# Performance work log

Hardware: AMD Instinct MI355X
Metric: run time of the kernel (lower is better)

The kernel has to match this reference:

```python
import jax, jax.numpy as jnp
import numpy as np

VOCAB, EMBED, CONT, HID = 829, 8, 40, 32
B, T, CODES = 2048, 256, 32
IN_DIM = EMBED + CONT + 1  # 49: embedding-sum + continuous feats + vanco feedback
SCALE = 1000.0  # all four regularizer scales


def setup_inputs() -> dict:
    key = jax.random.key(0)
    ks = jax.random.split(key, 14)
    s = 1.0 / np.sqrt(HID)
    return {
        "cont": jax.random.normal(ks[0], (B, T, CONT), jnp.float32),
        "cat": jax.random.randint(ks[1], (B, T, CODES), 0, VOCAB),
        "lb": jax.random.uniform(ks[2], (B, T), jnp.float32),
        "dose": jax.random.uniform(ks[3], (B, T), jnp.float32),
        "td": jax.random.uniform(ks[4], (B, T), jnp.float32),
        "v_from_weight": jax.random.uniform(ks[5], (B, T), jnp.float32) + 0.5,
        "vanco_el": jax.random.uniform(ks[6], (B, T), jnp.float32),
        "embed": jax.random.normal(ks[7], (VOCAB, EMBED), jnp.float32) * 0.02,
        "W_ih": jax.random.uniform(ks[8], (3 * HID, IN_DIM), jnp.float32, -s, s),
        "W_hh": jax.random.uniform(ks[9], (3 * HID, HID), jnp.float32, -s, s),
        "b_ih": jax.random.uniform(ks[10], (3 * HID,), jnp.float32, -s, s),
        "b_hh": jax.random.uniform(ks[11], (3 * HID,), jnp.float32, -s, s),
        "W_out": jax.random.uniform(ks[12], (2, HID), jnp.float32, -s, s),
        "b_out": jax.random.uniform(ks[13], (2,), jnp.float32, -s, s),
    }


def _gru_cell(x, h, W_ih, W_hh, b_ih, b_hh):
    gi = x @ W_ih.T + b_ih  # [B, 3H]
    gh = h @ W_hh.T + b_hh
    i_r, i_z, i_n = jnp.split(gi, 3, axis=1)
    h_r, h_z, h_n = jnp.split(gh, 3, axis=1)
    r = jax.nn.sigmoid(i_r + h_r)
    z = jax.nn.sigmoid(i_z + h_z)
    n = jnp.tanh(i_n + r * h_n)
    return (1.0 - z) * n + z * h


def reference(cont, cat, lb, dose, td, v_from_weight, vanco_el,
              embed, W_ih, W_hh, b_ih, b_hh, W_out, b_out):
    dt = cont.dtype
    mask = (lb != 0).astype(dt)  # [B, T]
    # EHR embedding: sum code embeddings per step, concat continuous features
    out_emb = jnp.concatenate([embed[cat].sum(axis=2), cont], axis=2)  # [B, T, 48]
    Bn, Tn = lb.shape
    # feedback uses previous step's mask/label (zeros at step 0)
    fm = jnp.concatenate([jnp.zeros((Bn, 1), dt), mask[:, :-1]], axis=1)
    fl = jnp.concatenate([jnp.zeros((Bn, 1), dt), lb[:, :-1]], axis=1)

    def step(carry, xs):
        h, tm, prev_concn = carry
        e_t, fm_t, fl_t, d_t, td_t = xs
        vfb = jax.lax.stop_gradient(prev_concn) * (1.0 - fm_t) + fl_t * fm_t
        x = jnp.concatenate([e_t, vfb[:, None]], axis=1)  # [B, 49]
        h2 = _gru_cell(x, h, W_ih, W_hh, b_ih, b_hh)
        kv = jnp.exp(h2 @ W_out.T + b_out)  # [B, 2]
        k, v = kv[:, 0], kv[:, 1]
        A = jnp.exp(-k * td_t)
        Bq = (1.0 / k) * (1.0 - jnp.exp(-k * d_t)) * jnp.exp(-k * (td_t - d_t))
        tm2 = tm * A + Bq
        concn = tm2 / (v + 1e-6)
        return (h2, tm2, concn), (concn, k, v)

    init = (jnp.zeros((Bn, HID), dt), jnp.zeros((Bn,), dt), jnp.zeros((Bn,), dt))
    xs = (out_emb.transpose(1, 0, 2), fm.T, fl.T, dose.T, td.T)
    _, (concn, K, V) = jax.lax.scan(step, init, xs)
    output, K, V = concn.T, K.T, V.T  # [B, T]

    kv_change = ((K[:, 1:] - K[:, :-1]) ** 2).mean() * SCALE \
              + ((V[:, 1:] - V[:, :-1]) ** 2).mean() * SCALE
    mse_loss = (((output - lb) * mask) ** 2).sum() / mask.sum()
    K0, V0 = vanco_el[:, 0], v_from_weight[:, 0]
    loss = mse_loss + ((K0 - K[:, 0]) ** 2).mean() * SCALE \
                    + ((V0 - V[:, 0]) ** 2).mean() * SCALE + kv_change
    return (K, V, output, loss, mse_loss)
```

## Files before the change

kernel.cpp:

```cpp
#include <hip/hip_runtime.h>


constexpr int Bn = 2048, Tn = 256;
constexpr int HID = 32, CONT = 40, EMB = 8;
constexpr int VOCAB = 829, CODES = 32;
constexpr int BT = Bn * Tn;
constexpr int LOSS_BLOCKS = 256;

__device__ __forceinline__ float frcp(float x) { return __builtin_amdgcn_rcpf(x); }

__device__ __forceinline__ float swap_add(float x) {
  return x + __shfl_xor(x, 32, 64);
}

template <int CTRL>
__device__ __forceinline__ float dpp_add(float x) {
  int y = __builtin_amdgcn_update_dpp(0, __float_as_int(x), CTRL, 0xf, 0xf, true);
  return x + __int_as_float(y);
}

__global__ __launch_bounds__(256, 2) void rnn_kernel(
    const float* __restrict__ cont, const int* __restrict__ cat,
    const float* __restrict__ lb, const float* __restrict__ dose,
    const float* __restrict__ tdp, const float* __restrict__ embed,
    const float* __restrict__ W_ih, const float* __restrict__ W_hh,
    const float* __restrict__ b_ih, const float* __restrict__ b_hh,
    const float* __restrict__ W_out, const float* __restrict__ b_out,
    float* __restrict__ out) {
  __shared__ __attribute__((aligned(16))) float esh[VOCAB * EMB];
  __shared__ __attribute__((aligned(16))) float ebl[4][64][EMB];
  __shared__ __attribute__((aligned(16))) float hsh[4][HID];

  const int tid = threadIdx.x;
  const int wv = tid >> 6;
  const int j = tid & 63;
  const int u = j & 31;
  const int half = j >> 5;
  const int b = blockIdx.x * 4 + wv;
  const int base = b * Tn;

  for (int i = tid; i < VOCAB * EMB; i += 256) esh[i] = embed[i];
  __syncthreads();

  float wxr[24], wxz[24], wxn[24];
  {
    const float* Wr = W_ih + (size_t)u * 49;
    const float* Wz = W_ih + (size_t)(HID + u) * 49;
    const float* Wn = W_ih + (size_t)(2 * HID + u) * 49;
    const int eo = half * 4;
    const int co = 8 + half * 20;
#pragma unroll
    for (int k = 0; k < 4; k++) { wxr[k] = Wr[eo + k]; wxz[k] = Wz[eo + k]; wxn[k] = Wn[eo + k]; }
#pragma unroll
    for (int k = 0; k < 20; k++) {
      wxr[4 + k] = Wr[co + k]; wxz[4 + k] = Wz[co + k]; wxn[4 + k] = Wn[co + k];
    }
  }
  const float wvr = half ? W_ih[(size_t)u * 49 + 48] : 0.0f;
  const float wvz = half ? W_ih[(size_t)(HID + u) * 49 + 48] : 0.0f;
  const float wvn = half ? W_ih[(size_t)(2 * HID + u) * 49 + 48] : 0.0f;
  float whr[16], whz[16], whn[16];
#pragma unroll
  for (int k = 0; k < 16; k++) {
    whr[k] = W_hh[(size_t)u * HID + half * 16 + k];
    whz[k] = W_hh[(size_t)(HID + u) * HID + half * 16 + k];
    whn[k] = W_hh[(size_t)(2 * HID + u) * HID + half * 16 + k];
  }
  const float br = half ? 0.0f : (b_ih[u] + b_hh[u]);
  const float bz = half ? 0.0f : (b_ih[HID + u] + b_hh[HID + u]);
  const float bni = half ? 0.0f : b_ih[2 * HID + u];
  const float bnh = half ? 0.0f : b_hh[2 * HID + u];
  const float wkv = W_out[half * HID + u];
  const float bo0 = b_out[0], bo1 = b_out[1];

  hsh[wv][u] = 0.0f;
  float hj = 0.0f, tm = 0.0f, concn = 0.0f;
  float td_c = tdp[base], d_c = dose[base], lbp_c = 0.0f;

  float4 xA[5], xB[5];
  {
    const float4* c4 = reinterpret_cast<const float4*>(cont + (size_t)base * CONT + half * 20);
#pragma unroll
    for (int q = 0; q < 5; q++) xA[q] = c4[q];
  }

#define STEP(XC, XN, TT)                                                          \
  {                                                                               \
    const int t = (TT);                                                           \
    const int tn = (t + 1 < Tn) ? (t + 1) : t;                                    \
    {                                              \
      const float4* c4 = reinterpret_cast<const float4*>(                         \
          cont + (size_t)(base + tn) * CONT + half * 20);                         \
      _Pragma("unroll") for (int q = 0; q < 5; q++) XN[q] = c4[q];                \
    }                                                                             \
    const float td_n = tdp[base + tn];                                            \
    const float d_n = dose[base + tn];                                            \
    const float lbp_n = lb[base + tn - 1];                                        \
    const float4 e = *reinterpret_cast<const float4*>(&ebl[wv][t & 63][half * 4]);\
    float ar = wxr[0] * e.x + wxr[1] * e.y + wxr[2] * e.z + wxr[3] * e.w;         \
    float az = wxz[0] * e.x + wxz[1] * e.y + wxz[2] * e.z + wxz[3] * e.w;         \
    float an = wxn[0] * e.x + wxn[1] * e.y + wxn[2] * e.z + wxn[3] * e.w;         \
    _Pragma("unroll") for (int q = 0; q < 5; q++) {                               \
      const float4 xv = XC[q];                                                    \
      const int k0 = 4 + q * 4;                                                   \
      ar += wxr[k0] * xv.x + wxr[k0 + 1] * xv.y + wxr[k0 + 2] * xv.z +            \
            wxr[k0 + 3] * xv.w;                                                   \
      az += wxz[k0] * xv.x + wxz[k0 + 1] * xv.y + wxz[k0 + 2] * xv.z +            \
            wxz[k0 + 3] * xv.w;                                                   \
      an += wxn[k0] * xv.x + wxn[k0 + 1] * xv.y + wxn[k0 + 2] * xv.z +            \
            wxn[k0 + 3] * xv.w;                                                   \
    }                                                                             \
    float gr, gz, gn;                                                             \
    {                                                                             \
      const float4* h4 = reinterpret_cast<const float4*>(&hsh[wv][half * 16]);    \
      const float4 h0 = h4[0];                                                    \
      gr = whr[0] * h0.x + whr[1] * h0.y + whr[2] * h0.z + whr[3] * h0.w;         \
      gz = whz[0] * h0.x + whz[1] * h0.y + whz[2] * h0.z + whz[3] * h0.w;         \
      gn = whn[0] * h0.x + whn[1] * h0.y + whn[2] * h0.z + whn[3] * h0.w;         \
      _Pragma("unroll") for (int q = 1; q < 4; q++) {                             \
        const float4 hv = h4[q];                                                  \
        const int k0 = q * 4;                                                     \
        gr += whr[k0] * hv.x + whr[k0 + 1] * hv.y + whr[k0 + 2] * hv.z +          \
              whr[k0 + 3] * hv.w;                                                 \
        gz += whz[k0] * hv.x + whz[k0 + 1] * hv.y + whz[k0 + 2] * hv.z +          \
              whz[k0 + 3] * hv.w;                                                 \
        gn += whn[k0] * hv.x + whn[k0 + 1] * hv.y + whn[k0 + 2] * hv.z +          \
              whn[k0 + 3] * hv.w;                                                 \
      }                                                                           \
    }                                                                             \
    const float fmv = (lbp_c != 0.0f) ? 1.0f : 0.0f;                              \
    const float vfb = concn * (1.0f - fmv) + lbp_c * fmv;                         \
    ar += vfb * wvr;                                                              \
    az += vfb * wvz;                                                              \
    an += vfb * wvn;                                                              \
    const float sr = swap_add(ar + gr + br);                                      \
    const float sz = swap_add(az + gz + bz);                                      \
    const float sa = swap_add(an + bni);                                          \
    const float sg = swap_add(gn + bnh);                                          \
    const float r = frcp(1.0f + __expf(-sr));                                     \
    const float z = frcp(1.0f + __expf(-sz));                                     \
    const float pre = sa + r * sg;                                                \
    const float nv = 1.0f - 2.0f * frcp(__expf(2.0f * pre) + 1.0f);               \
    const float h2 = (1.0f - z) * nv + z * hj;                                    \
    hsh[wv][u] = h2;                                                              \
    hj = h2;                                                                      \
           \
    float s = h2 * wkv;                                                           \
    s = dpp_add<0x111>(s);                                         \
    s = dpp_add<0x112>(s);                                         \
    s = dpp_add<0x114>(s);                                         \
    s = dpp_add<0x118>(s);                                         \
    s = dpp_add<0x142>(s);  \
    const float pk_s = __int_as_float(__builtin_amdgcn_readlane(__float_as_int(s), 31)); \
    const float pv_s = __int_as_float(__builtin_amdgcn_readlane(__float_as_int(s), 63)); \
    const float kk = __expf(pk_s + bo0);                                          \
    const float vv = __expf(pv_s + bo1);                                          \
    const float Aa = __expf(-kk * td_c);                                          \
    const float eD = __expf(-kk * d_c);                                           \
    const float Bq = frcp(kk) * (1.0f - eD) * __expf(-kk * (td_c - d_c));         \
    tm = tm * Aa + Bq;                                                            \
    concn = tm * frcp(vv + 1e-6f);                                                \
    if (j < 3) {                                                                  \
      const float val = (j == 0) ? kk : ((j == 1) ? vv : concn);                  \
      out[j * BT + base + t] = val;                                               \
    }                                                                             \
    td_c = td_n;                                                                  \
    d_c = d_n;                                                                    \
    lbp_c = lbp_n;                                                                \
  }

  for (int ch = 0; ch < Tn / 64; ++ch) {
    {
      const int4* cp4 =
          reinterpret_cast<const int4*>(cat + ((size_t)(base + ch * 64 + j)) * CODES);
      float a0 = 0.f, a1 = 0.f, a2 = 0.f, a3 = 0.f;
      float a4 = 0.f, a5 = 0.f, a6 = 0.f, a7 = 0.f;
#pragma unroll
      for (int q = 0; q < 8; q++) {
        const int4 c4 = cp4[q];
        {
          const float4* er = reinterpret_cast<const float4*>(esh + c4.x * EMB);
          const float4 r0 = er[0], r1 = er[1];
          a0 += r0.x; a1 += r0.y; a2 += r0.z; a3 += r0.w;
          a4 += r1.x; a5 += r1.y; a6 += r1.z; a7 += r1.w;
        }
        {
          const float4* er = reinterpret_cast<const float4*>(esh + c4.y * EMB);
          const float4 r0 = er[0], r1 = er[1];
          a0 += r0.x; a1 += r0.y; a2 += r0.z; a3 += r0.w;
          a4 += r1.x; a5 += r1.y; a6 += r1.z; a7 += r1.w;
        }
        {
          const float4* er = reinterpret_cast<const float4*>(esh + c4.z * EMB);
          const float4 r0 = er[0], r1 = er[1];
          a0 += r0.x; a1 += r0.y; a2 += r0.z; a3 += r0.w;
          a4 += r1.x; a5 += r1.y; a6 += r1.z; a7 += r1.w;
        }
        {
          const float4* er = reinterpret_cast<const float4*>(esh + c4.w * EMB);
          const float4 r0 = er[0], r1 = er[1];
          a0 += r0.x; a1 += r0.y; a2 += r0.z; a3 += r0.w;
          a4 += r1.x; a5 += r1.y; a6 += r1.z; a7 += r1.w;
        }
      }
      *reinterpret_cast<float4*>(&ebl[wv][j][0]) = make_float4(a0, a1, a2, a3);
      *reinterpret_cast<float4*>(&ebl[wv][j][4]) = make_float4(a4, a5, a6, a7);
    }
    __syncthreads();
#pragma unroll 1
    for (int tl = 0; tl < 64; tl += 2) {
      STEP(xA, xB, ch * 64 + tl);
      STEP(xB, xA, ch * 64 + tl + 1);
    }
  }
#undef STEP
}

__global__ __launch_bounds__(256) void loss_partial_kernel(
    const float* __restrict__ out, const float* __restrict__ lb,
    const float* __restrict__ vel, const float* __restrict__ vfw,
    float* __restrict__ part) {
  float mseN = 0.f, cnt = 0.f, k0 = 0.f, v0 = 0.f, dk = 0.f, dv = 0.f;
  for (int i = blockIdx.x * 256 + threadIdx.x; i < BT; i += LOSS_BLOCKS * 256) {
    const int t = i & (Tn - 1);
    const float l = lb[i];
    const float m = (l != 0.0f) ? 1.0f : 0.0f;
    const float c = out[2 * BT + i];
    const float d = (c - l) * m;
    mseN += d * d;
    cnt += m;
    const float kc = out[i];
    const float vc = out[BT + i];
    if (t > 0) {
      const float kp = out[i - 1];
      const float vp = out[BT + i - 1];
      dk += (kc - kp) * (kc - kp);
      dv += (vc - vp) * (vc - vp);
    } else {
      const float a = vel[i] - kc;
      const float bb = vfw[i] - vc;
      k0 += a * a;
      v0 += bb * bb;
    }
  }
  float acc[6] = {mseN, cnt, k0, v0, dk, dv};
#pragma unroll
  for (int q = 0; q < 6; q++) {
#pragma unroll
    for (int mm = 1; mm < 64; mm <<= 1) acc[q] += __shfl_xor(acc[q], mm, 64);
  }
  __shared__ float red[4][6];
  if ((threadIdx.x & 63) == 0) {
#pragma unroll
    for (int q = 0; q < 6; q++) red[threadIdx.x >> 6][q] = acc[q];
  }
  __syncthreads();
  if (threadIdx.x == 0) {
#pragma unroll
    for (int q = 0; q < 6; q++)
      part[blockIdx.x * 6 + q] = red[0][q] + red[1][q] + red[2][q] + red[3][q];
  }
}

__device__ __forceinline__ void finalize_loss(const float s[6], float* out) {
  const float mse = s[0] / s[1];
  const float loss = mse + (s[2] / (float)Bn) * 1000.0f + (s[3] / (float)Bn) * 1000.0f +
                     (s[4] / (float)(Bn * (Tn - 1))) * 1000.0f +
                     (s[5] / (float)(Bn * (Tn - 1))) * 1000.0f;
  out[3 * BT] = loss;
  out[3 * BT + 1] = mse;
}

__global__ __launch_bounds__(256) void loss_final_kernel(const float* __restrict__ part,
                                                         float* __restrict__ out) {
  float acc[6] = {0.f, 0.f, 0.f, 0.f, 0.f, 0.f};
  for (int i = threadIdx.x; i < LOSS_BLOCKS; i += 256) {
#pragma unroll
    for (int q = 0; q < 6; q++) acc[q] += part[i * 6 + q];
  }
#pragma unroll
  for (int q = 0; q < 6; q++) {
#pragma unroll
    for (int mm = 1; mm < 64; mm <<= 1) acc[q] += __shfl_xor(acc[q], mm, 64);
  }
  __shared__ float red[4][6];
  if ((threadIdx.x & 63) == 0) {
#pragma unroll
    for (int q = 0; q < 6; q++) red[threadIdx.x >> 6][q] = acc[q];
  }
  __syncthreads();
  if (threadIdx.x == 0) {
    float s[6];
#pragma unroll
    for (int q = 0; q < 6; q++) s[q] = red[0][q] + red[1][q] + red[2][q] + red[3][q];
    finalize_loss(s, out);
  }
}

__global__ __launch_bounds__(1024) void loss_single_kernel(
    const float* __restrict__ out, const float* __restrict__ lb,
    const float* __restrict__ vel, const float* __restrict__ vfw,
    float* __restrict__ outw) {
  float mseN = 0.f, cnt = 0.f, k0 = 0.f, v0 = 0.f, dk = 0.f, dv = 0.f;
  for (int i = threadIdx.x; i < BT; i += 1024) {
    const int t = i & (Tn - 1);
    const float l = lb[i];
    const float m = (l != 0.0f) ? 1.0f : 0.0f;
    const float c = out[2 * BT + i];
    const float d = (c - l) * m;
    mseN += d * d;
    cnt += m;
    const float kc = out[i];
    const float vc = out[BT + i];
    if (t > 0) {
      const float kp = out[i - 1];
      const float vp = out[BT + i - 1];
      dk += (kc - kp) * (kc - kp);
      dv += (vc - vp) * (vc - vp);
    } else {
      const float a = vel[i] - kc;
      const float bb = vfw[i] - vc;
      k0 += a * a;
      v0 += bb * bb;
    }
  }
  float acc[6] = {mseN, cnt, k0, v0, dk, dv};
#pragma unroll
  for (int q = 0; q < 6; q++) {
#pragma unroll
    for (int mm = 1; mm < 64; mm <<= 1) acc[q] += __shfl_xor(acc[q], mm, 64);
  }
  __shared__ float red[16][6];
  if ((threadIdx.x & 63) == 0) {
#pragma unroll
    for (int q = 0; q < 6; q++) red[threadIdx.x >> 6][q] = acc[q];
  }
  __syncthreads();
  if (threadIdx.x == 0) {
    float s[6] = {0.f, 0.f, 0.f, 0.f, 0.f, 0.f};
    for (int w = 0; w < 16; w++)
#pragma unroll
      for (int q = 0; q < 6; q++) s[q] += red[w][q];
    finalize_loss(s, outw);
  }
}

extern "C" void kernel_launch(void* const* d_in, const int* in_sizes, int n_in,
                              void* d_out, int out_size, void* d_ws, size_t ws_size,
                              hipStream_t stream) {
  (void)in_sizes; (void)n_in; (void)out_size;
  const float* cont = (const float*)d_in[0];
  const int* cat = (const int*)d_in[1];
  const float* lb = (const float*)d_in[2];
  const float* dose = (const float*)d_in[3];
  const float* tdp = (const float*)d_in[4];
  const float* vfw = (const float*)d_in[5];
  const float* vel = (const float*)d_in[6];
  const float* emb = (const float*)d_in[7];
  const float* W_ih = (const float*)d_in[8];
  const float* W_hh = (const float*)d_in[9];
  const float* b_ih = (const float*)d_in[10];
  const float* b_hh = (const float*)d_in[11];
  const float* W_out = (const float*)d_in[12];
  const float* b_out = (const float*)d_in[13];
  float* out = (float*)d_out;

  rnn_kernel<<<Bn / 4, 256, 0, stream>>>(cont, cat, lb, dose, tdp, emb, W_ih, W_hh,
                                         b_ih, b_hh, W_out, b_out, out);

  if (d_ws != nullptr && ws_size >= (size_t)LOSS_BLOCKS * 6 * sizeof(float)) {
    float* part = (float*)d_ws;
    loss_partial_kernel<<<LOSS_BLOCKS, 256, 0, stream>>>(out, lb, vel, vfw, part);
    loss_final_kernel<<<1, 256, 0, stream>>>(part, out);
  } else {
    loss_single_kernel<<<1, 1024, 0, stream>>>(out, lb, vel, vfw, out);
  }
}
```

Baseline: 237.7 us.

## Deepen input prefetch to two steps and batch per-step outputs through LDS

The recurrent loop now prefetches continuous features and the scalar inputs two timesteps ahead, using four rotating register buffers and a four-step unrolled loop, so global load latency is hidden further behind the serial recurrence. Per-step scalar stores of k, v and concentration from three lanes are replaced by writes into a shared buffer. Each 64-step chunk is then flushed with one coalesced store per output. This adds register pressure under the 2-blocks-per-SM launch bound, plus extra LDS use.

```diff
diff --git a/kernel.cpp b/kernel.cpp
--- a/kernel.cpp
+++ b/kernel.cpp
@@ -30,6 +30,7 @@
   __shared__ __attribute__((aligned(16))) float esh[VOCAB * EMB];
   __shared__ __attribute__((aligned(16))) float ebl[4][64][EMB];
   __shared__ __attribute__((aligned(16))) float hsh[4][HID];
+  __shared__ __attribute__((aligned(16))) float osh[4][3][64];
 
   const int tid = threadIdx.x;
   const int wv = tid >> 6;
@@ -75,33 +76,36 @@
 
   hsh[wv][u] = 0.0f;
   float hj = 0.0f, tm = 0.0f, concn = 0.0f;
+
   float td_c = tdp[base], d_c = dose[base], lbp_c = 0.0f;
-
-  float4 xA[5], xB[5];
+  float td_1 = tdp[base + 1], d_1 = dose[base + 1], lbp_1 = lb[base];
+
+  float4 xA[5], xB[5], xC[5], xD[5];
   {
-    const float4* c4 = reinterpret_cast<const float4*>(cont + (size_t)base * CONT + half * 20);
-#pragma unroll
-    for (int q = 0; q < 5; q++) xA[q] = c4[q];
-  }
-
-#define STEP(XC, XN, TT)                                                          \
+    const float4* c0 = reinterpret_cast<const float4*>(cont + (size_t)base * CONT + half * 20);
+    const float4* c1 = reinterpret_cast<const float4*>(cont + (size_t)(base + 1) * CONT + half * 20);
+#pragma unroll
+    for (int q = 0; q < 5; q++) { xA[q] = c0[q]; xB[q] = c1[q]; }
+  }
+
+#define STEP(XC_, XP_, TT)                                                        \
   {                                                                               \
     const int t = (TT);                                                           \
-    const int tn = (t + 1 < Tn) ? (t + 1) : t;                                    \
+    const int tn2 = (t + 2 < Tn) ? (t + 2) : (Tn - 1);                            \
     {                                              \
       const float4* c4 = reinterpret_cast<const float4*>(                         \
-          cont + (size_t)(base + tn) * CONT + half * 20);                         \
-      _Pragma("unroll") for (int q = 0; q < 5; q++) XN[q] = c4[q];                \
+          cont + (size_t)(base + tn2) * CONT + half * 20);                        \
+      _Pragma("unroll") for (int q = 0; q < 5; q++) XP_[q] = c4[q];               \
     }                                                                             \
-    const float td_n = tdp[base + tn];                                            \
-    const float d_n = dose[base + tn];                                            \
-    const float lbp_n = lb[base + tn - 1];                                        \
+    const float td_2 = tdp[base + tn2];                                           \
+    const float d_2 = dose[base + tn2];                                           \
+    const float lbp_2 = lb[base + tn2 - 1];                                       \
     const float4 e = *reinterpret_cast<const float4*>(&ebl[wv][t & 63][half * 4]);\
     float ar = wxr[0] * e.x + wxr[1] * e.y + wxr[2] * e.z + wxr[3] * e.w;         \
     float az = wxz[0] * e.x + wxz[1] * e.y + wxz[2] * e.z + wxz[3] * e.w;         \
     float an = wxn[0] * e.x + wxn[1] * e.y + wxn[2] * e.z + wxn[3] * e.w;         \
     _Pragma("unroll") for (int q = 0; q < 5; q++) {                               \
-      const float4 xv = XC[q];                                                    \
+      const float4 xv = XC_[q];                                                   \
       const int k0 = 4 + q * 4;                                                   \
       ar += wxr[k0] * xv.x + wxr[k0 + 1] * xv.y + wxr[k0 + 2] * xv.z +            \
             wxr[k0 + 3] * xv.w;                                                   \
@@ -144,13 +148,13 @@
     const float h2 = (1.0f - z) * nv + z * hj;                                    \
     hsh[wv][u] = h2;                                                              \
     hj = h2;                                                                      \
-           \
+                          \
     float s = h2 * wkv;                                                           \
     s = dpp_add<0x111>(s);                                         \
     s = dpp_add<0x112>(s);                                         \
     s = dpp_add<0x114>(s);                                         \
     s = dpp_add<0x118>(s);                                         \
-    s = dpp_add<0x142>(s);  \
+    s = dpp_add<0x142>(s);                                      \
     const float pk_s = __int_as_float(__builtin_amdgcn_readlane(__float_as_int(s), 31)); \
     const float pv_s = __int_as_float(__builtin_amdgcn_readlane(__float_as_int(s), 63)); \
     const float kk = __expf(pk_s + bo0);                                          \
@@ -160,13 +164,13 @@
     const float Bq = frcp(kk) * (1.0f - eD) * __expf(-kk * (td_c - d_c));         \
     tm = tm * Aa + Bq;                                                            \
     concn = tm * frcp(vv + 1e-6f);                                                \
-    if (j < 3) {                                                                  \
+    if (j < 3) {                    \
       const float val = (j == 0) ? kk : ((j == 1) ? vv : concn);                  \
-      out[j * BT + base + t] = val;                                               \
+      osh[wv][j][t & 63] = val;                                                   \
     }                                                                             \
-    td_c = td_n;                                                                  \
-    d_c = d_n;                                                                    \
-    lbp_c = lbp_n;                                                                \
+    td_c = td_1; td_1 = td_2;                                                     \
+    d_c = d_1;  d_1 = d_2;                                                        \
+    lbp_c = lbp_1; lbp_1 = lbp_2;                                                 \
   }
 
   for (int ch = 0; ch < Tn / 64; ++ch) {
@@ -208,10 +212,14 @@
     }
     __syncthreads();
 #pragma unroll 1
-    for (int tl = 0; tl < 64; tl += 2) {
-      STEP(xA, xB, ch * 64 + tl);
-      STEP(xB, xA, ch * 64 + tl + 1);
-    }
+    for (int tl = 0; tl < 64; tl += 4) {
+      STEP(xA, xC, ch * 64 + tl);
+      STEP(xB, xD, ch * 64 + tl + 1);
+      STEP(xC, xA, ch * 64 + tl + 2);
+      STEP(xD, xB, ch * 64 + tl + 3);
+    }
+#pragma unroll
+    for (int q = 0; q < 3; q++) out[q * BT + base + ch * 64 + j] = osh[wv][q][j];
   }
 #undef STEP
 }
```

New measurement: 241.0 us. About the same (+1.4%).
